# Optimization experiments

Hardware: AMD Instinct MI355X
Metric: run time of the kernel (lower is better)

Reference implementation:

```python
import jax, jax.numpy as jnp
import numpy as np

N_NODES = 100000
N_EDGES = 3200000
K_STEPS = 10
ALPHA = 0.1


def setup_inputs() -> dict:
    key = jax.random.key(0)
    k = jax.random.split(key, 6)
    x = jax.random.normal(k[0], (N_NODES, 512), dtype=jnp.float32)
    W1 = jax.random.normal(k[1], (256, 512), dtype=jnp.float32) * (1.0 / np.sqrt(512))
    b1 = jnp.zeros((256,), dtype=jnp.float32)
    W2 = jax.random.normal(k[2], (16, 256), dtype=jnp.float32) * (1.0 / np.sqrt(256))
    b2 = jnp.zeros((16,), dtype=jnp.float32)
    edge_index = jax.random.randint(k[3], (2, N_EDGES), 0, N_NODES, dtype=jnp.int64)
    return {"x": x, "W1": W1, "b1": b1, "W2": W2, "b2": b2, "edge_index": edge_index}


def reference(x, W1, b1, W2, b2, edge_index):
    N = x.shape[0]
    # MLP preamble (dropout inactive at inference)
    h = jax.nn.relu(x @ W1.T + b1) @ W2.T + b2  # [N, classes]

    # gcn_norm with self-loops: A_hat = D^-1/2 (A + I) D^-1/2
    loop = jnp.arange(N, dtype=edge_index.dtype)
    src = jnp.concatenate([edge_index[0], loop])
    dst = jnp.concatenate([edge_index[1], loop])
    deg = jax.ops.segment_sum(jnp.ones(src.shape[0], dtype=h.dtype), dst, num_segments=N)
    dinv = jnp.where(deg > 0, jax.lax.rsqrt(deg), 0.0)
    norm = dinv[src] * dinv[dst]  # [E+N]

    def step(z, _):
        msg = z[src] * norm[:, None]  # gather + scale
        agg = jax.ops.segment_sum(msg, dst, num_segments=N)  # scatter-add
        return (1.0 - ALPHA) * agg + ALPHA * h, None

    z, _ = jax.lax.scan(step, h, None, length=K_STEPS)
    return jax.nn.log_softmax(z, axis=1)
```

## Files before the change

### kernel.cpp

```cpp
#include <hip/hip_runtime.h>
#include <hip/hip_bf16.h>
#include <stdint.h>

#define N_NODES 100000
#define N_EDGES 3200000
#define ALPHA   0.1f

typedef __attribute__((ext_vector_type(8))) short v8s;
typedef __attribute__((ext_vector_type(4))) float f32x4;

__device__ __forceinline__ uint32_t bf16_rne(float f) {
    uint32_t u = __float_as_uint(f);
    return (u + 0x7FFFu + ((u >> 16) & 1u)) >> 16;
}
__device__ __forceinline__ float bf16_f32(uint32_t b) { return __uint_as_float(b << 16); }

__global__ __launch_bounds__(256) void w1_frag_kernel(
    const float* __restrict__ W1, uint4* __restrict__ W1f)
{
    int tid = blockIdx.x * 256 + threadIdx.x;
    int ks = tid >> 10, T = (tid >> 6) & 15, l = tid & 63;
    int row = T * 16 + (l & 15);
    int kb  = ks * 32 + (l >> 4) * 8;
    const float* src = W1 + (size_t)row * 512 + kb;
    float4 f0 = *(const float4*)(src);
    float4 f1 = *(const float4*)(src + 4);
    float f[8] = {f0.x, f0.y, f0.z, f0.w, f1.x, f1.y, f1.z, f1.w};
    uint32_t hi[8], lo[8];
#pragma unroll
    for (int j = 0; j < 8; ++j) {
        hi[j] = bf16_rne(f[j]);
        lo[j] = bf16_rne(f[j] - bf16_f32(hi[j]));
    }
    uint4 H = make_uint4(hi[0] | (hi[1] << 16), hi[2] | (hi[3] << 16),
                         hi[4] | (hi[5] << 16), hi[6] | (hi[7] << 16));
    uint4 L = make_uint4(lo[0] | (lo[1] << 16), lo[2] | (lo[3] << 16),
                         lo[4] | (lo[5] << 16), lo[6] | (lo[7] << 16));
    size_t base = ((size_t)(ks * 2) * 16 + T) * 64 + l;
    W1f[base]        = H;
    W1f[base + 1024] = L;
}

__global__ __launch_bounds__(256, 2) void mlp_kernel(
    const float* __restrict__ x, const uint4* __restrict__ W1f,
    const float* __restrict__ b1, const float* __restrict__ W2,
    const float* __restrict__ b2, const float* __restrict__ dinv,
    float* __restrict__ h, float* __restrict__ hs, int n)
{
    __shared__ __align__(16) char smem[33280];
    char*  xs   = smem;
    float* W2s  = (float*)smem;
    float* part = (float*)(smem + 16640);

    const int tid = threadIdx.x;
    const int w = tid >> 6, l = tid & 63;
    const int l15 = l & 15, q = l >> 4;
    const int row0 = blockIdx.x * 64;

    const int s_l15 = tid & 15;
    const int s_seg = (tid >> 4) & 3;
    const int s_u   = tid >> 6;
    const int s_grow = row0 + s_u * 16 + s_l15;

    f32x4 acc[4][4];
#pragma unroll
    for (int mt = 0; mt < 4; ++mt)
#pragma unroll
        for (int nt = 0; nt < 4; ++nt) acc[mt][nt] = (f32x4){0.f, 0.f, 0.f, 0.f};

    for (int ks = 0; ks < 16; ++ks) {
        uint4 aHu[4], aLu[4];
#pragma unroll
        for (int mt = 0; mt < 4; ++mt) {
            size_t cidx = ((size_t)(ks * 2) * 16 + (w * 4 + mt)) * 64 + l;
            aHu[mt] = W1f[cidx];
            aLu[mt] = W1f[cidx + 1024];
        }
        float4 f0 = make_float4(0.f, 0.f, 0.f, 0.f), f1 = f0;
        if (s_grow < n) {
            const float* xp = x + (size_t)s_grow * 512 + ks * 32 + s_seg * 8;
            f0 = *(const float4*)(xp);
            f1 = *(const float4*)(xp + 4);
        }
        float f[8] = {f0.x, f0.y, f0.z, f0.w, f1.x, f1.y, f1.z, f1.w};
        uint32_t hi[8], lo[8];
#pragma unroll
        for (int j = 0; j < 8; ++j) {
            hi[j] = bf16_rne(f[j]);
            lo[j] = bf16_rne(f[j] - bf16_f32(hi[j]));
        }
        uint4 H = make_uint4(hi[0] | (hi[1] << 16), hi[2] | (hi[3] << 16),
                             hi[4] | (hi[5] << 16), hi[6] | (hi[7] << 16));
        uint4 L = make_uint4(lo[0] | (lo[1] << 16), lo[2] | (lo[3] << 16),
                             lo[4] | (lo[5] << 16), lo[6] | (lo[7] << 16));
        __syncthreads();
        *(uint4*)(xs +        s_u * 1024 + (s_seg * 16 + s_l15) * 16) = H;
        *(uint4*)(xs + 4096 + s_u * 1024 + (s_seg * 16 + s_l15) * 16) = L;
        __syncthreads();

        v8s bH[4], bL[4];
#pragma unroll
        for (int nt = 0; nt < 4; ++nt) {
            bH[nt] = *(v8s*)(xs +        nt * 1024 + l * 16);
            bL[nt] = *(v8s*)(xs + 4096 + nt * 1024 + l * 16);
        }
#pragma unroll
        for (int mt = 0; mt < 4; ++mt) {
            v8s aH = *(v8s*)&aHu[mt];
            v8s aL = *(v8s*)&aLu[mt];
#pragma unroll
            for (int nt = 0; nt < 4; ++nt) {
                f32x4 c = acc[mt][nt];
                c = __builtin_amdgcn_mfma_f32_16x16x32_bf16(aH, bH[nt], c, 0, 0, 0);
                c = __builtin_amdgcn_mfma_f32_16x16x32_bf16(aH, bL[nt], c, 0, 0, 0);
                c = __builtin_amdgcn_mfma_f32_16x16x32_bf16(aL, bH[nt], c, 0, 0, 0);
                acc[mt][nt] = c;
            }
        }
    }

#pragma unroll
    for (int mt = 0; mt < 4; ++mt) {
        float4 bv = *(const float4*)(b1 + w * 64 + mt * 16 + q * 4);
#pragma unroll
        for (int nt = 0; nt < 4; ++nt) {
            acc[mt][nt][0] = fmaxf(acc[mt][nt][0] + bv.x, 0.f);
            acc[mt][nt][1] = fmaxf(acc[mt][nt][1] + bv.y, 0.f);
            acc[mt][nt][2] = fmaxf(acc[mt][nt][2] + bv.z, 0.f);
            acc[mt][nt][3] = fmaxf(acc[mt][nt][3] + bv.w, 0.f);
        }
    }

    __syncthreads();
    {
        int c = tid >> 4, k16 = (tid & 15) * 16;
#pragma unroll
        for (int i = 0; i < 4; ++i)
            *(float4*)(W2s + c * 260 + k16 + i * 4) =
                *(const float4*)(W2 + c * 256 + k16 + i * 4);
    }
    __syncthreads();

#pragma unroll
    for (int c4 = 0; c4 < 4; ++c4) {
        float p2[4][4];
#pragma unroll
        for (int nt = 0; nt < 4; ++nt)
#pragma unroll
            for (int cc = 0; cc < 4; ++cc) p2[nt][cc] = 0.f;
#pragma unroll
        for (int mt = 0; mt < 4; ++mt)
#pragma unroll
            for (int cc = 0; cc < 4; ++cc) {
                float4 wv = *(float4*)(W2s + (c4 * 4 + cc) * 260 + w * 64 + mt * 16 + q * 4);
#pragma unroll
                for (int nt = 0; nt < 4; ++nt)
                    p2[nt][cc] += acc[mt][nt][0] * wv.x + acc[mt][nt][1] * wv.y +
                                  acc[mt][nt][2] * wv.z + acc[mt][nt][3] * wv.w;
            }
#pragma unroll
        for (int nt = 0; nt < 4; ++nt)
#pragma unroll
            for (int cc = 0; cc < 4; ++cc) {
                p2[nt][cc] += __shfl_xor(p2[nt][cc], 16);
                p2[nt][cc] += __shfl_xor(p2[nt][cc], 32);
            }
        if (q == c4) {
#pragma unroll
            for (int nt = 0; nt < 4; ++nt)
                *(float4*)(part + ((w * 64 + nt * 16 + l15) << 4) + c4 * 4) =
                    make_float4(p2[nt][0], p2[nt][1], p2[nt][2], p2[nt][3]);
        }
    }
    __syncthreads();
    {
        int node = tid >> 2, c4 = (tid & 3) * 4;
        float4 s = make_float4(0.f, 0.f, 0.f, 0.f);
#pragma unroll
        for (int ww = 0; ww < 4; ++ww) {
            float4 v = *(float4*)(part + ((ww * 64 + node) << 4) + c4);
            s.x += v.x; s.y += v.y; s.z += v.z; s.w += v.w;
        }
        float4 bv = *(const float4*)(b2 + c4);
        int grow = row0 + node;
        if (grow < n) {
            float4 hv = make_float4(s.x + bv.x, s.y + bv.y, s.z + bv.z, s.w + bv.w);
            *(float4*)(h + (size_t)grow * 16 + c4) = hv;
            float di = dinv[grow];
            *(float4*)(hs + (size_t)grow * 16 + c4) =
                make_float4(di * hv.x, di * hv.y, di * hv.z, di * hv.w);
        }
    }
}

__global__ void hist_kernel(const int* __restrict__ dst, int* __restrict__ cnt, int e)
{
    int i = blockIdx.x * blockDim.x + threadIdx.x;
    if (i < e) atomicAdd(&cnt[dst[i]], 1);
}

__global__ void dinv_kernel(const int* __restrict__ cnt, float* __restrict__ dinv,
                            int* __restrict__ pcnt,
                            float* __restrict__ zsA_dummy, float* __restrict__ zsB_dummy,
                            int n)
{
    int i = blockIdx.x * blockDim.x + threadIdx.x;
    if (i < n) {
        int c = cnt[i];
        dinv[i] = rsqrtf((float)c + 1.0f);
        pcnt[i] = (c + 15) & ~15;
    }
    if (i < 16) { zsA_dummy[i] = 0.0f; zsB_dummy[i] = 0.0f; }
}

__global__ void fill_kernel(int4* __restrict__ p, int v, int cnt4)
{
    int i = blockIdx.x * blockDim.x + threadIdx.x;
    if (i < cnt4) p[i] = make_int4(v, v, v, v);
}

__global__ __launch_bounds__(256) void scan1_kernel(
    const int* __restrict__ pcnt, int* __restrict__ row_loc,
    int* __restrict__ bsum, int n)
{
    __shared__ int sm[256];
    int i = blockIdx.x * 256 + threadIdx.x;
    int v = (i < n) ? pcnt[i] : 0;
    sm[threadIdx.x] = v;
    __syncthreads();
#pragma unroll
    for (int off = 1; off < 256; off <<= 1) {
        int t = (threadIdx.x >= off) ? sm[threadIdx.x - off] : 0;
        __syncthreads();
        sm[threadIdx.x] += t;
        __syncthreads();
    }
    if (i <= n) row_loc[i] = sm[threadIdx.x] - v;
    if (threadIdx.x == 255) bsum[blockIdx.x] = sm[255];
}

__global__ __launch_bounds__(512) void scan2_kernel(
    const int* __restrict__ bsum, int* __restrict__ boff, int nb)
{
    __shared__ int sm[512];
    int i = threadIdx.x;
    int v = (i < nb) ? bsum[i] : 0;
    sm[i] = v;
    __syncthreads();
#pragma unroll
    for (int off = 1; off < 512; off <<= 1) {
        int t = (i >= off) ? sm[i - off] : 0;
        __syncthreads();
        sm[i] += t;
        __syncthreads();
    }
    if (i < nb) boff[i] = sm[i] - v;
}

__global__ void scan3_kernel(int* __restrict__ row_st, const int* __restrict__ boff,
                             int* __restrict__ cursor, int n)
{
    int i = blockIdx.x * blockDim.x + threadIdx.x;
    if (i <= n) {
        int r = row_st[i] + boff[i >> 8];
        row_st[i] = r;
        if (i < n) cursor[i] = r;
    }
}

#define SC_CHUNK 2048
__global__ __launch_bounds__(256) void scatter8_kernel(
    const int* __restrict__ src, const int* __restrict__ dst,
    int* __restrict__ cursor, int* __restrict__ csr_s, int e)
{
    const int w    = blockIdx.x & 7;
    const int base = (blockIdx.x >> 3) * SC_CHUNK;
    const int wlo  = w * (N_NODES / 8);
    const int whi  = wlo + (N_NODES / 8);
#pragma unroll
    for (int t = 0; t < SC_CHUNK / 256; ++t) {
        int i = base + t * 256 + threadIdx.x;
        if (i < e) {
            int d = dst[i];
            if (d >= wlo && d < whi) {
                int s = src[i];
                int pos = atomicAdd(&cursor[d], 1);
                csr_s[pos] = s;
            }
        }
    }
}

__global__ __launch_bounds__(256) void prop_kernel(
    const int* __restrict__ csr_s, const int* __restrict__ row_st,
    const float* __restrict__ dinv, const float* __restrict__ zs_in,
    const float* __restrict__ hmat, float* __restrict__ out,
    int n, int is_last)
{
    const int t = threadIdx.x;
    const int d = blockIdx.x * 16 + (t >> 4);
    if (d >= n) return;
    const int lane16 = t & 15;
    const int sub = lane16 >> 2;
    const int f4 = (lane16 & 3) * 4;
    const int rs = row_st[d], re = row_st[d + 1];

    float4 S = make_float4(0.f, 0.f, 0.f, 0.f);
    int j = rs + sub * 4;
    for (; j + 16 < re; j += 32) {
        int4 s0 = *(const int4*)(csr_s + j);
        int4 s1 = *(const int4*)(csr_s + j + 16);
        const float4 a0 = *(const float4*)(zs_in + (size_t)s0.x * 16 + f4);
        const float4 b0 = *(const float4*)(zs_in + (size_t)s0.y * 16 + f4);
        const float4 c0 = *(const float4*)(zs_in + (size_t)s0.z * 16 + f4);
        const float4 e0 = *(const float4*)(zs_in + (size_t)s0.w * 16 + f4);
        const float4 a1 = *(const float4*)(zs_in + (size_t)s1.x * 16 + f4);
        const float4 b1 = *(const float4*)(zs_in + (size_t)s1.y * 16 + f4);
        const float4 c1 = *(const float4*)(zs_in + (size_t)s1.z * 16 + f4);
        const float4 e1 = *(const float4*)(zs_in + (size_t)s1.w * 16 + f4);
        S.x += ((a0.x + b0.x) + (c0.x + e0.x)) + ((a1.x + b1.x) + (c1.x + e1.x));
        S.y += ((a0.y + b0.y) + (c0.y + e0.y)) + ((a1.y + b1.y) + (c1.y + e1.y));
        S.z += ((a0.z + b0.z) + (c0.z + e0.z)) + ((a1.z + b1.z) + (c1.z + e1.z));
        S.w += ((a0.w + b0.w) + (c0.w + e0.w)) + ((a1.w + b1.w) + (c1.w + e1.w));
    }
    if (j < re) {
        int4 s0 = *(const int4*)(csr_s + j);
        const float4 a0 = *(const float4*)(zs_in + (size_t)s0.x * 16 + f4);
        const float4 b0 = *(const float4*)(zs_in + (size_t)s0.y * 16 + f4);
        const float4 c0 = *(const float4*)(zs_in + (size_t)s0.z * 16 + f4);
        const float4 e0 = *(const float4*)(zs_in + (size_t)s0.w * 16 + f4);
        S.x += (a0.x + b0.x) + (c0.x + e0.x);
        S.y += (a0.y + b0.y) + (c0.y + e0.y);
        S.z += (a0.z + b0.z) + (c0.z + e0.z);
        S.w += (a0.w + b0.w) + (c0.w + e0.w);
    }

    S.x += __shfl_xor(S.x, 4); S.y += __shfl_xor(S.y, 4);
    S.z += __shfl_xor(S.z, 4); S.w += __shfl_xor(S.w, 4);
    S.x += __shfl_xor(S.x, 8); S.y += __shfl_xor(S.y, 8);
    S.z += __shfl_xor(S.z, 8); S.w += __shfl_xor(S.w, 8);

    const float4 self = *(const float4*)(zs_in + (size_t)d * 16 + f4);
    S.x += self.x; S.y += self.y; S.z += self.z; S.w += self.w;

    const float di = dinv[d];
    const float4 hv = *(const float4*)(hmat + (size_t)d * 16 + f4);
    float4 zn;
    zn.x = fmaf(1.0f - ALPHA, di * S.x, ALPHA * hv.x);
    zn.y = fmaf(1.0f - ALPHA, di * S.y, ALPHA * hv.y);
    zn.z = fmaf(1.0f - ALPHA, di * S.z, ALPHA * hv.z);
    zn.w = fmaf(1.0f - ALPHA, di * S.w, ALPHA * hv.w);
    if (!is_last) {
        if (sub == 0)
            *(float4*)(out + (size_t)d * 16 + f4) =
                make_float4(di * zn.x, di * zn.y, di * zn.z, di * zn.w);
    } else {
        float m = fmaxf(fmaxf(zn.x, zn.y), fmaxf(zn.z, zn.w));
        m = fmaxf(m, __shfl_xor(m, 1));
        m = fmaxf(m, __shfl_xor(m, 2));
        float ss = expf(zn.x - m) + expf(zn.y - m) + expf(zn.z - m) + expf(zn.w - m);
        ss += __shfl_xor(ss, 1);
        ss += __shfl_xor(ss, 2);
        float ls = logf(ss);
        if (sub == 0)
            *(float4*)(out + (size_t)d * 16 + f4) =
                make_float4(zn.x - m - ls, zn.y - m - ls, zn.z - m - ls, zn.w - m - ls);
    }
}

extern "C" void kernel_launch(void* const* d_in, const int* in_sizes, int n_in,
                              void* d_out, int out_size, void* d_ws, size_t ws_size,
                              hipStream_t stream)
{
    const float* x  = (const float*)d_in[0];
    const float* W1 = (const float*)d_in[1];
    const float* b1 = (const float*)d_in[2];
    const float* W2 = (const float*)d_in[3];
    const float* b2 = (const float*)d_in[4];
    const int*   ei = (const int*)d_in[5];

    const int N = N_NODES;
    const int E = N_EDGES;
    const int EP_MAX = 4800000;
    const int* srcp = ei;
    const int* dstp = ei + E;

    float* ws = (float*)d_ws;
    float* h       = ws;
    float* ZSA     = ws + 1600000;
    float* ZSB     = ws + 3200016;
    float* dinv    = ws + 4800032;
    int*   row_st  = (int*)(ws + 4900032);
    int*   csr_s   = (int*)(ws + 5000036);
    int*   cnt     = (int*)(ws);
    int*   cursor  = (int*)(ws + 100000);
    int*   bsum    = (int*)(ws + 200000);
    int*   boff    = (int*)(ws + 200512);
    int*   pcnt    = (int*)(ws + 201024);
    uint4* W1f     = (uint4*)(ws + 1600000);
    float* zsA_dummy = ZSA + (size_t)N * 16;
    float* zsB_dummy = ZSB + (size_t)N * 16;

    const int NB_SCAN = (N + 255) / 256;

    hipMemsetAsync(cnt, 0, (size_t)N * sizeof(int), stream);
    hist_kernel<<<(E + 255) / 256, 256, 0, stream>>>(dstp, cnt, E);
    dinv_kernel<<<(N + 255) / 256, 256, 0, stream>>>(cnt, dinv, pcnt,
                                                     zsA_dummy, zsB_dummy, N);
    fill_kernel<<<(EP_MAX / 4 + 255) / 256, 256, 0, stream>>>((int4*)csr_s, N, EP_MAX / 4);
    scan1_kernel<<<NB_SCAN, 256, 0, stream>>>(pcnt, row_st, bsum, N);
    scan2_kernel<<<1, 512, 0, stream>>>(bsum, boff, NB_SCAN);
    scan3_kernel<<<(N + 256) / 256, 256, 0, stream>>>(row_st, boff, cursor, N);
    {
        const int nchunks = (E + SC_CHUNK - 1) / SC_CHUNK;
        scatter8_kernel<<<nchunks * 8, 256, 0, stream>>>(srcp, dstp, cursor, csr_s, E);
    }
    w1_frag_kernel<<<64, 256, 0, stream>>>(W1, W1f);
    mlp_kernel<<<(N + 63) / 64, 256, 0, stream>>>(x, W1f, b1, W2, b2, dinv, h, ZSB, N);

    const int NB_PROP = (N + 15) / 16;
    for (int k = 0; k < 10; ++k) {
        const int last = (k == 9) ? 1 : 0;
        const float* zin = (k == 0) ? ZSB : ((k & 1) ? ZSA : ZSB);
        float* zo = last ? (float*)d_out : ((k & 1) ? ZSB : ZSA);
        prop_kernel<<<NB_PROP, 256, 0, stream>>>(csr_s, row_st, dinv, zin, h, zo,
                                                 N, last);
    }
}
```

Measured before the change: 977.2 us.

## Prefetch x tiles, add low-low bf16 MFMA term, accumulate propagation in double

The MLP kernel now loads the next x slice into registers before the MFMA block of the current step, so global load latency overlaps with compute. It also adds a fourth lo*lo bf16 MFMA per tile, which raises split-bf16 accuracy at about a third more matrix work. The propagation kernel now sums gathered neighbours in double precision, including the shuffles, which costs FP64 add throughput and more registers. Taken together this mixes one latency-hiding idea with two accuracy-driven changes that add work.

```diff
diff --git a/kernel.cpp b/kernel.cpp
--- a/kernel.cpp
+++ b/kernel.cpp
@@ -61,12 +61,20 @@
     const int s_seg = (tid >> 4) & 3;
     const int s_u   = tid >> 6;
     const int s_grow = row0 + s_u * 16 + s_l15;
+    const bool s_ok = (s_grow < n);
+    const float* xrow = x + (size_t)s_grow * 512 + s_seg * 8;
 
     f32x4 acc[4][4];
 #pragma unroll
     for (int mt = 0; mt < 4; ++mt)
 #pragma unroll
         for (int nt = 0; nt < 4; ++nt) acc[mt][nt] = (f32x4){0.f, 0.f, 0.f, 0.f};
+
+    float4 f0 = make_float4(0.f, 0.f, 0.f, 0.f), f1 = f0;
+    if (s_ok) {
+        f0 = *(const float4*)(xrow);
+        f1 = *(const float4*)(xrow + 4);
+    }
 
     for (int ks = 0; ks < 16; ++ks) {
         uint4 aHu[4], aLu[4];
@@ -76,12 +84,6 @@
             aHu[mt] = W1f[cidx];
             aLu[mt] = W1f[cidx + 1024];
         }
-        float4 f0 = make_float4(0.f, 0.f, 0.f, 0.f), f1 = f0;
-        if (s_grow < n) {
-            const float* xp = x + (size_t)s_grow * 512 + ks * 32 + s_seg * 8;
-            f0 = *(const float4*)(xp);
-            f1 = *(const float4*)(xp + 4);
-        }
         float f[8] = {f0.x, f0.y, f0.z, f0.w, f1.x, f1.y, f1.z, f1.w};
         uint32_t hi[8], lo[8];
 #pragma unroll
@@ -97,6 +99,12 @@
         *(uint4*)(xs +        s_u * 1024 + (s_seg * 16 + s_l15) * 16) = H;
         *(uint4*)(xs + 4096 + s_u * 1024 + (s_seg * 16 + s_l15) * 16) = L;
         __syncthreads();
+
+        if (ks < 15 && s_ok) {
+            const float* xp = xrow + (ks + 1) * 32;
+            f0 = *(const float4*)(xp);
+            f1 = *(const float4*)(xp + 4);
+        }
 
         v8s bH[4], bL[4];
 #pragma unroll
@@ -114,6 +122,7 @@
                 c = __builtin_amdgcn_mfma_f32_16x16x32_bf16(aH, bH[nt], c, 0, 0, 0);
                 c = __builtin_amdgcn_mfma_f32_16x16x32_bf16(aH, bL[nt], c, 0, 0, 0);
                 c = __builtin_amdgcn_mfma_f32_16x16x32_bf16(aL, bH[nt], c, 0, 0, 0);
+                c = __builtin_amdgcn_mfma_f32_16x16x32_bf16(aL, bL[nt], c, 0, 0, 0);
                 acc[mt][nt] = c;
             }
         }
@@ -305,7 +314,7 @@
     const int f4 = (lane16 & 3) * 4;
     const int rs = row_st[d], re = row_st[d + 1];
 
-    float4 S = make_float4(0.f, 0.f, 0.f, 0.f);
+    double Sx = 0.0, Sy = 0.0, Sz = 0.0, Sw = 0.0;
     int j = rs + sub * 4;
     for (; j + 16 < re; j += 32) {
         int4 s0 = *(const int4*)(csr_s + j);
@@ -318,10 +327,14 @@
         const float4 b1 = *(const float4*)(zs_in + (size_t)s1.y * 16 + f4);
         const float4 c1 = *(const float4*)(zs_in + (size_t)s1.z * 16 + f4);
         const float4 e1 = *(const float4*)(zs_in + (size_t)s1.w * 16 + f4);
-        S.x += ((a0.x + b0.x) + (c0.x + e0.x)) + ((a1.x + b1.x) + (c1.x + e1.x));
-        S.y += ((a0.y + b0.y) + (c0.y + e0.y)) + ((a1.y + b1.y) + (c1.y + e1.y));
-        S.z += ((a0.z + b0.z) + (c0.z + e0.z)) + ((a1.z + b1.z) + (c1.z + e1.z));
-        S.w += ((a0.w + b0.w) + (c0.w + e0.w)) + ((a1.w + b1.w) + (c1.w + e1.w));
+        Sx += (((double)a0.x + (double)b0.x) + ((double)c0.x + (double)e0.x))
+            + (((double)a1.x + (double)b1.x) + ((double)c1.x + (double)e1.x));
+        Sy += (((double)a0.y + (double)b0.y) + ((double)c0.y + (double)e0.y))
+            + (((double)a1.y + (double)b1.y) + ((double)c1.y + (double)e1.y));
+        Sz += (((double)a0.z + (double)b0.z) + ((double)c0.z + (double)e0.z))
+            + (((double)a1.z + (double)b1.z) + ((double)c1.z + (double)e1.z));
+        Sw += (((double)a0.w + (double)b0.w) + ((double)c0.w + (double)e0.w))
+            + (((double)a1.w + (double)b1.w) + ((double)c1.w + (double)e1.w));
     }
     if (j < re) {
         int4 s0 = *(const int4*)(csr_s + j);
@@ -329,19 +342,21 @@
         const float4 b0 = *(const float4*)(zs_in + (size_t)s0.y * 16 + f4);
         const float4 c0 = *(const float4*)(zs_in + (size_t)s0.z * 16 + f4);
         const float4 e0 = *(const float4*)(zs_in + (size_t)s0.w * 16 + f4);
-        S.x += (a0.x + b0.x) + (c0.x + e0.x);
-        S.y += (a0.y + b0.y) + (c0.y + e0.y);
-        S.z += (a0.z + b0.z) + (c0.z + e0.z);
-        S.w += (a0.w + b0.w) + (c0.w + e0.w);
-    }
-
-    S.x += __shfl_xor(S.x, 4); S.y += __shfl_xor(S.y, 4);
-    S.z += __shfl_xor(S.z, 4); S.w += __shfl_xor(S.w, 4);
-    S.x += __shfl_xor(S.x, 8); S.y += __shfl_xor(S.y, 8);
-    S.z += __shfl_xor(S.z, 8); S.w += __shfl_xor(S.w, 8);
+        Sx += ((double)a0.x + (double)b0.x) + ((double)c0.x + (double)e0.x);
+        Sy += ((double)a0.y + (double)b0.y) + ((double)c0.y + (double)e0.y);
+        Sz += ((double)a0.z + (double)b0.z) + ((double)c0.z + (double)e0.z);
+        Sw += ((double)a0.w + (double)b0.w) + ((double)c0.w + (double)e0.w);
+    }
+
+    Sx += __shfl_xor(Sx, 4); Sy += __shfl_xor(Sy, 4);
+    Sz += __shfl_xor(Sz, 4); Sw += __shfl_xor(Sw, 4);
+    Sx += __shfl_xor(Sx, 8); Sy += __shfl_xor(Sy, 8);
+    Sz += __shfl_xor(Sz, 8); Sw += __shfl_xor(Sw, 8);
 
     const float4 self = *(const float4*)(zs_in + (size_t)d * 16 + f4);
-    S.x += self.x; S.y += self.y; S.z += self.z; S.w += self.w;
+    Sx += (double)self.x; Sy += (double)self.y;
+    Sz += (double)self.z; Sw += (double)self.w;
+    float4 S = make_float4((float)Sx, (float)Sy, (float)Sz, (float)Sw);
 
     const float di = dinv[d];
     const float4 hv = *(const float4*)(hmat + (size_t)d * 16 + f4);
```

After: 997.0 us. 1.02x slower.
